# Kernel optimization log

Measured on AMD Instinct MI355X. Metric: run time of the kernel, lower is better.

Reference implementation:

```python
import jax, jax.numpy as jnp
import numpy as np

B, N, D, H, DH, DEPTH, VOCAB, MULT = 4, 1024, 768, 12, 64, 6, 32000, 4
INNER = H * DH
FF = D * MULT
EPS = 1e-6


def setup_inputs() -> dict:
    key = jax.random.key(0)
    ks = jax.random.split(key, 9)
    s = lambda fan: 1.0 / np.sqrt(fan)
    return {
        "tokens": jax.random.randint(ks[0], (B, N), 0, VOCAB, dtype=jnp.int32),
        "mask": jnp.ones((B, N), dtype=bool),
        "embed": jax.random.normal(ks[1], (VOCAB, D), jnp.float32),
        "wq": jax.random.normal(ks[2], (DEPTH, INNER, D), jnp.float32) * s(D),
        "wk": jax.random.normal(ks[3], (DEPTH, INNER, D), jnp.float32) * s(D),
        "wv": jax.random.normal(ks[4], (DEPTH, INNER, D), jnp.float32) * s(D),
        "wo": jax.random.normal(ks[5], (DEPTH, D, INNER), jnp.float32) * s(INNER),
        "wi": jax.random.normal(ks[6], (DEPTH, FF, D), jnp.float32) * s(D),
        "wof": jax.random.normal(ks[7], (DEPTH, D, FF), jnp.float32) * s(FF),
        "ln_w": jnp.ones((D,), jnp.float32),
    }


def _t5_layernorm(x, w):
    var = jnp.mean(jnp.square(x.astype(jnp.float32)), axis=-1, keepdims=True)
    return w * (x * jax.lax.rsqrt(var + EPS))


def reference(tokens, mask, embed, wq, wk, wv, wo, wi, wof, ln_w):
    x = embed[tokens]  # [B, N, D]
    scale = DH ** -0.5
    neg = -jnp.finfo(x.dtype).max
    m = mask[:, None, :, None]  # masks query rows, as in the torch code
    for l in range(DEPTH):
        # attention (no pre-LN: WrapperBlock never calls its layer_norm)
        q = (x @ wq[l].T).reshape(B, N, H, DH).transpose(0, 2, 1, 3) * scale
        k = (x @ wk[l].T).reshape(B, N, H, DH).transpose(0, 2, 1, 3)
        v = (x @ wv[l].T).reshape(B, N, H, DH).transpose(0, 2, 1, 3)
        sim = jnp.einsum('bhid,bhjd->bhij', q, k)
        sim = jnp.where(m, sim, neg)
        attn = jax.nn.softmax(sim, axis=-1)
        o = jnp.einsum('bhij,bhjd->bhid', attn, v)
        o = o.transpose(0, 2, 1, 3).reshape(B, N, INNER) @ wo[l].T
        x = x + o
        # feed-forward
        y = jax.nn.relu(x @ wi[l].T) @ wof[l].T
        x = x + y
    return _t5_layernorm(x, ln_w)
```

## Files before the change

### kernel.cpp

```cpp
#include <hip/hip_runtime.h>
#include <cstdint>

#define NB 4
#define NSEQ 1024
#define DMODEL 768
#define NHEAD 12
#define DHEAD 64
#define NDEPTH 6
#define DFF 3072
#define MROWS (NB * NSEQ)
#define QKVLD 2304

#define WQ_OFF 0L
#define WK_OFF 589824L
#define WV_OFF 1179648L
#define WO_OFF 1769472L
#define WI_OFF 2359296L
#define WOF_OFF 4718592L
#define WTOT 7077888L

typedef __attribute__((ext_vector_type(8))) short short8;
typedef __attribute__((ext_vector_type(4))) float floatx4;

static __device__ __forceinline__ float b2f(unsigned short u) {
  union { unsigned int i; float f; } v; v.i = ((unsigned int)u) << 16; return v.f;
}
static __device__ __forceinline__ unsigned short f2b(float f) {
  union { float f; unsigned int i; } v; v.f = f;
  unsigned int x = v.i;
  return (unsigned short)((x + 0x7fffu + ((x >> 16) & 1u)) >> 16);
}
static __device__ __forceinline__ void fsplit(float f, unsigned short& h, unsigned short& l) {
  h = f2b(f);
  l = f2b(f - b2f(h));
}

static __device__ __forceinline__ void gload16(const unsigned short* g, unsigned short* l) {
  __builtin_amdgcn_global_load_lds(
      (const __attribute__((address_space(1))) void*)g,
      (__attribute__((address_space(3))) void*)l, 16, 0, 0);
}

__global__ __launch_bounds__(256) void wsplit_kernel(
    const float* __restrict__ wq, const float* __restrict__ wk,
    const float* __restrict__ wv, const float* __restrict__ wo,
    const float* __restrict__ wi, const float* __restrict__ wof,
    unsigned short* __restrict__ dhi, unsigned short* __restrict__ dlo)
{
  long i = ((long)blockIdx.x * 256 + threadIdx.x) * 4;
  if (i >= WTOT) return;
  const float* src; long off;
  if (i < WK_OFF)       { src = wq;  off = i - WQ_OFF; }
  else if (i < WV_OFF)  { src = wk;  off = i - WK_OFF; }
  else if (i < WO_OFF)  { src = wv;  off = i - WV_OFF; }
  else if (i < WI_OFF)  { src = wo;  off = i - WO_OFF; }
  else if (i < WOF_OFF) { src = wi;  off = i - WI_OFF; }
  else                  { src = wof; off = i - WOF_OFF; }
  float4 f = *(const float4*)(src + off);
  ushort4 h, l;
  fsplit(f.x, h.x, l.x); fsplit(f.y, h.y, l.y);
  fsplit(f.z, h.z, l.z); fsplit(f.w, h.w, l.w);
  *(ushort4*)(dhi + i) = h;
  *(ushort4*)(dlo + i) = l;
}

__global__ void embed_kernel(const int* __restrict__ tok,
                             const float* __restrict__ emb,
                             unsigned short* __restrict__ xhi,
                             unsigned short* __restrict__ xlo) {
  const int row = blockIdx.x;
  const int t = tok[row];
  const float* src = emb + (long)t * DMODEL;
  for (int d = threadIdx.x; d < DMODEL; d += 256) {
    unsigned short h, l;
    fsplit(src[d], h, l);
    xhi[(long)row * DMODEL + d] = h;
    xlo[(long)row * DMODEL + d] = l;
  }
}

template<int BM, int WGM, int WGN, int MT, int NT, int RELU, int RESID, int QSCALE>
__global__ __launch_bounds__(256) void gemm128(
    const unsigned short* __restrict__ Ahi, const unsigned short* __restrict__ Alo,
    const unsigned short* __restrict__ Whi, const unsigned short* __restrict__ Wlo,
    unsigned short* __restrict__ Chi, unsigned short* __restrict__ Clo,
    const unsigned short* __restrict__ Rhi, const unsigned short* __restrict__ Rlo,
    int N, int K, float alpha)
{
  __shared__ unsigned short sAh[BM * 32];
  __shared__ unsigned short sAl[BM * 32];
  __shared__ unsigned short sBh[128 * 32];
  __shared__ unsigned short sBl[128 * 32];

  const int tid = threadIdx.x;
  const int bn = blockIdx.x, bm = blockIdx.y;
  const int wave = tid >> 6, lane = tid & 63;
  const int wm = wave / WGN, wn = wave % WGN;
  const int l16 = lane & 15, q4 = lane >> 4;

  const int srow = tid >> 2;
  const int scol = (tid & 3) << 3;
  const int soff = tid * 8;

  floatx4 acc[MT][NT];
  #pragma unroll
  for (int i = 0; i < MT; ++i)
    #pragma unroll
    for (int j = 0; j < NT; ++j) {
      floatx4 z = {0.f, 0.f, 0.f, 0.f};
      acc[i][j] = z;
    }

  const long aB = ((long)bm * BM + srow) * K + scol;
  const long bB = ((long)bn * 128 + srow) * K + scol;

  for (int k0 = 0; k0 < K; k0 += 32) {
    #pragma unroll
    for (int c = 0; c < BM / 64; ++c) {
      gload16(Ahi + aB + (long)c * 64 * K + k0, sAh + c * 2048 + soff);
      gload16(Alo + aB + (long)c * 64 * K + k0, sAl + c * 2048 + soff);
    }
    #pragma unroll
    for (int c = 0; c < 2; ++c) {
      gload16(Whi + bB + (long)c * 64 * K + k0, sBh + c * 2048 + soff);
      gload16(Wlo + bB + (long)c * 64 * K + k0, sBl + c * 2048 + soff);
    }
    __syncthreads();

    short8 ah[MT], al[MT], bh[NT], bl[NT];
    #pragma unroll
    for (int mt = 0; mt < MT; ++mt) {
      const int row = wm * (MT * 16) + mt * 16 + l16;
      ah[mt] = *(const short8*)&sAh[row * 32 + q4 * 8];
      al[mt] = *(const short8*)&sAl[row * 32 + q4 * 8];
    }
    #pragma unroll
    for (int nt = 0; nt < NT; ++nt) {
      const int row = wn * (NT * 16) + nt * 16 + l16;
      bh[nt] = *(const short8*)&sBh[row * 32 + q4 * 8];
      bl[nt] = *(const short8*)&sBl[row * 32 + q4 * 8];
    }

    #pragma unroll
    for (int mt = 0; mt < MT; ++mt)
      #pragma unroll
      for (int nt = 0; nt < NT; ++nt)
        acc[mt][nt] = __builtin_amdgcn_mfma_f32_16x16x32_bf16(ah[mt], bh[nt], acc[mt][nt], 0, 0, 0);
    #pragma unroll
    for (int mt = 0; mt < MT; ++mt)
      #pragma unroll
      for (int nt = 0; nt < NT; ++nt)
        acc[mt][nt] = __builtin_amdgcn_mfma_f32_16x16x32_bf16(al[mt], bh[nt], acc[mt][nt], 0, 0, 0);
    #pragma unroll
    for (int mt = 0; mt < MT; ++mt)
      #pragma unroll
      for (int nt = 0; nt < NT; ++nt)
        acc[mt][nt] = __builtin_amdgcn_mfma_f32_16x16x32_bf16(ah[mt], bl[nt], acc[mt][nt], 0, 0, 0);
    __syncthreads();
  }

  #pragma unroll
  for (int mt = 0; mt < MT; ++mt) {
    const int r0 = bm * BM + wm * (MT * 16) + mt * 16 + q4 * 4;
    #pragma unroll
    for (int nt = 0; nt < NT; ++nt) {
      const int c = bn * 128 + wn * (NT * 16) + nt * 16 + l16;
      float sc = alpha;
      if (QSCALE) sc = (c < DMODEL) ? alpha : 1.f;
      #pragma unroll
      for (int r = 0; r < 4; ++r) {
        float vv = acc[mt][nt][r] * sc;
        const long idx = (long)(r0 + r) * N + c;
        if (RESID) vv += b2f(Rhi[idx]) + b2f(Rlo[idx]);
        if (RELU)  vv = fmaxf(vv, 0.f);
        unsigned short h, l;
        fsplit(vv, h, l);
        Chi[idx] = h; Clo[idx] = l;
      }
    }
  }
}

__global__ __launch_bounds__(256) void attn_kernel(
    const unsigned short* __restrict__ qkvhi, const unsigned short* __restrict__ qkvlo,
    unsigned short* __restrict__ ohi, unsigned short* __restrict__ olo)
{
  __shared__ unsigned short ks_h[64][72];
  __shared__ unsigned short ks_l[64][72];
  __shared__ unsigned short vt_h[64][72];
  __shared__ unsigned short vt_l[64][72];
  __shared__ unsigned short ps_h[64][72];
  __shared__ unsigned short ps_l[64][72];

  const int tid = threadIdx.x;
  const int iq = blockIdx.x, h = blockIdx.y, b = blockIdx.z;
  const int wave = tid >> 6, lane = tid & 63;
  const int l16 = lane & 15, g4 = lane >> 4;
  const long qb = ((long)b * NSEQ) * QKVLD + h * DHEAD;
  const long kb = qb + DMODEL;
  const long vb = qb + 2 * DMODEL;
  const long ob = ((long)b * NSEQ) * DMODEL + h * DHEAD;
  const int q0 = iq * 64;

  short8 qh[2], ql[2];
  {
    const long qr = qb + (long)(q0 + wave * 16 + l16) * QKVLD + g4 * 8;
    qh[0] = *(const short8*)(qkvhi + qr);
    qh[1] = *(const short8*)(qkvhi + qr + 32);
    ql[0] = *(const short8*)(qkvlo + qr);
    ql[1] = *(const short8*)(qkvlo + qr + 32);
  }

  floatx4 oacc[4];
  #pragma unroll
  for (int nt = 0; nt < 4; ++nt) { floatx4 z = {0.f,0.f,0.f,0.f}; oacc[nt] = z; }
  float mrow[4] = {-INFINITY, -INFINITY, -INFINITY, -INFINITY};
  float lrow[4] = {0.f, 0.f, 0.f, 0.f};

  const int skey = tid >> 3;
  const int sd0  = (tid & 7) * 8;

  for (int jc = 0; jc < NSEQ / 64; ++jc) {
    const int j0 = jc * 64;
    if (jc) __syncthreads();

    #pragma unroll
    for (int half = 0; half < 2; ++half) {
      const int key = skey + half * 32;
      const long offk = kb + (long)(j0 + key) * QKVLD + sd0;
      const long offv = vb + (long)(j0 + key) * QKVLD + sd0;
      short8 kh8 = *(const short8*)(qkvhi + offk);
      short8 kl8 = *(const short8*)(qkvlo + offk);
      short8 vh8 = *(const short8*)(qkvhi + offv);
      short8 vl8 = *(const short8*)(qkvlo + offv);
      *(short8*)&ks_h[key][sd0] = kh8;
      *(short8*)&ks_l[key][sd0] = kl8;
      #pragma unroll
      for (int u = 0; u < 8; ++u) {
        const int dh = sd0 + u;
        const int cc = key ^ ((dh >> 3) << 3);
        vt_h[dh][cc] = (unsigned short)vh8[u];
        vt_l[dh][cc] = (unsigned short)vl8[u];
      }
    }
    __syncthreads();

    floatx4 sacc[4];
    #pragma unroll
    for (int nt = 0; nt < 4; ++nt) { floatx4 z = {0.f,0.f,0.f,0.f}; sacc[nt] = z; }
    #pragma unroll
    for (int nt = 0; nt < 4; ++nt) {
      #pragma unroll
      for (int ks = 0; ks < 2; ++ks) {
        short8 kh8 = *(const short8*)&ks_h[nt * 16 + l16][ks * 32 + g4 * 8];
        short8 kl8 = *(const short8*)&ks_l[nt * 16 + l16][ks * 32 + g4 * 8];
        sacc[nt] = __builtin_amdgcn_mfma_f32_16x16x32_bf16(qh[ks], kh8, sacc[nt], 0, 0, 0);
        sacc[nt] = __builtin_amdgcn_mfma_f32_16x16x32_bf16(ql[ks], kh8, sacc[nt], 0, 0, 0);
        sacc[nt] = __builtin_amdgcn_mfma_f32_16x16x32_bf16(qh[ks], kl8, sacc[nt], 0, 0, 0);
      }
    }

    float mx[4], al[4];
    #pragma unroll
    for (int r = 0; r < 4; ++r) {
      float m0 = fmaxf(fmaxf(sacc[0][r], sacc[1][r]), fmaxf(sacc[2][r], sacc[3][r]));
      m0 = fmaxf(m0, __shfl_xor(m0, 1));
      m0 = fmaxf(m0, __shfl_xor(m0, 2));
      m0 = fmaxf(m0, __shfl_xor(m0, 4));
      m0 = fmaxf(m0, __shfl_xor(m0, 8));
      const float mn = fmaxf(mrow[r], m0);
      al[r] = __expf(mrow[r] - mn);
      mrow[r] = mn;
      mx[r] = mn;
    }
    #pragma unroll
    for (int r = 0; r < 4; ++r) {
      const int qrow = wave * 16 + g4 * 4 + r;
      float rs = 0.f;
      #pragma unroll
      for (int nt = 0; nt < 4; ++nt) {
        const float p = __expf(sacc[nt][r] - mx[r]);
        rs += p;
        unsigned short ph, pl;
        fsplit(p, ph, pl);
        ps_h[qrow][nt * 16 + l16] = ph;
        ps_l[qrow][nt * 16 + l16] = pl;
      }
      rs += __shfl_xor(rs, 1);
      rs += __shfl_xor(rs, 2);
      rs += __shfl_xor(rs, 4);
      rs += __shfl_xor(rs, 8);
      lrow[r] = lrow[r] * al[r] + rs;
      oacc[0][r] *= al[r]; oacc[1][r] *= al[r];
      oacc[2][r] *= al[r]; oacc[3][r] *= al[r];
    }
    __syncthreads();

    #pragma unroll
    for (int ks = 0; ks < 2; ++ks) {
      short8 ph8 = *(const short8*)&ps_h[wave * 16 + l16][ks * 32 + g4 * 8];
      short8 pl8 = *(const short8*)&ps_l[wave * 16 + l16][ks * 32 + g4 * 8];
      #pragma unroll
      for (int nt = 0; nt < 4; ++nt) {
        const int dh = nt * 16 + l16;
        const int cb = (ks * 32 + g4 * 8) ^ ((dh >> 3) << 3);
        short8 vh8 = *(const short8*)&vt_h[dh][cb];
        short8 vl8 = *(const short8*)&vt_l[dh][cb];
        oacc[nt] = __builtin_amdgcn_mfma_f32_16x16x32_bf16(ph8, vh8, oacc[nt], 0, 0, 0);
        oacc[nt] = __builtin_amdgcn_mfma_f32_16x16x32_bf16(pl8, vh8, oacc[nt], 0, 0, 0);
        oacc[nt] = __builtin_amdgcn_mfma_f32_16x16x32_bf16(ph8, vl8, oacc[nt], 0, 0, 0);
      }
    }
  }

  const long orbase = ob + (long)(q0 + wave * 16 + g4 * 4) * DMODEL;
  #pragma unroll
  for (int r = 0; r < 4; ++r) {
    const float inv = 1.f / lrow[r];
    #pragma unroll
    for (int nt = 0; nt < 4; ++nt) {
      unsigned short hh, ll;
      fsplit(oacc[nt][r] * inv, hh, ll);
      const long idx = orbase + (long)r * DMODEL + nt * 16 + l16;
      ohi[idx] = hh; olo[idx] = ll;
    }
  }
}

__global__ __launch_bounds__(256) void ln_kernel(const unsigned short* __restrict__ xhi,
                                                 const unsigned short* __restrict__ xlo,
                                                 const float* __restrict__ w,
                                                 float* __restrict__ out)
{
  __shared__ float red[256];
  const int row = blockIdx.x;
  const long rb = (long)row * DMODEL;
  float ss = 0.f;
  for (int d = threadIdx.x; d < DMODEL; d += 256) {
    float v = b2f(xhi[rb + d]) + b2f(xlo[rb + d]);
    ss += v * v;
  }
  red[threadIdx.x] = ss;
  __syncthreads();
  for (int s = 128; s > 0; s >>= 1) {
    if (threadIdx.x < s) red[threadIdx.x] += red[threadIdx.x + s];
    __syncthreads();
  }
  const float rs = rsqrtf(red[0] * (1.f / DMODEL) + 1e-6f);
  for (int d = threadIdx.x; d < DMODEL; d += 256) {
    float v = b2f(xhi[rb + d]) + b2f(xlo[rb + d]);
    out[rb + d] = w[d] * v * rs;
  }
}

extern "C" void kernel_launch(void* const* d_in, const int* in_sizes, int n_in,
                              void* d_out, int out_size, void* d_ws, size_t ws_size,
                              hipStream_t stream)
{
  const int* tokens   = (const int*)d_in[0];
  const float* emb    = (const float*)d_in[2];
  const float* wq     = (const float*)d_in[3];
  const float* wk     = (const float*)d_in[4];
  const float* wv     = (const float*)d_in[5];
  const float* wo     = (const float*)d_in[6];
  const float* wi     = (const float*)d_in[7];
  const float* wof    = (const float*)d_in[8];
  const float* lnw    = (const float*)d_in[9];

  const size_t AS = (size_t)MROWS * DMODEL;
  char* p = (char*)d_ws;
  unsigned short* xhi = (unsigned short*)p;  p += AS * 2;
  unsigned short* xlo = (unsigned short*)p;  p += AS * 2;
  unsigned short* act = (unsigned short*)p;  p += AS * 2 * 8;
  unsigned short* whi = (unsigned short*)p;  p += (size_t)WTOT * 2;
  unsigned short* wlo = (unsigned short*)p;  p += (size_t)WTOT * 2;

  unsigned short* qkvhi = act + AS * 0;
  unsigned short* qkvlo = act + AS * 3;
  unsigned short* ohi   = act + AS * 6;
  unsigned short* olo   = act + AS * 7;
  unsigned short* fhi   = act + AS * 0;
  unsigned short* flo   = act + AS * 4;

  embed_kernel<<<MROWS, 256, 0, stream>>>(tokens, emb, xhi, xlo);

  const dim3 gqkv(QKVLD / 128, MROWS / 128);
  const dim3 gwo(DMODEL / 128, MROWS / 64);
  const dim3 gwi(DFF / 128, MROWS / 128);
  const dim3 gattn(NSEQ / 64, NHEAD, NB);
  const int splitblocks = (int)(WTOT / 1024);

  for (int l = 0; l < NDEPTH; ++l) {
    wsplit_kernel<<<splitblocks, 256, 0, stream>>>(
        wq  + (size_t)l * DMODEL * DMODEL,
        wk  + (size_t)l * DMODEL * DMODEL,
        wv  + (size_t)l * DMODEL * DMODEL,
        wo  + (size_t)l * DMODEL * DMODEL,
        wi  + (size_t)l * DFF * DMODEL,
        wof + (size_t)l * DMODEL * DFF,
        whi, wlo);

    gemm128<128,2,2,4,4, 0,0,1><<<gqkv, 256, 0, stream>>>(
        xhi, xlo, whi + WQ_OFF, wlo + WQ_OFF,
        qkvhi, qkvlo, nullptr, nullptr, QKVLD, DMODEL, 0.125f);
    attn_kernel<<<gattn, 256, 0, stream>>>(qkvhi, qkvlo, ohi, olo);
    gemm128<64,1,4,4,2, 0,1,0><<<gwo, 256, 0, stream>>>(
        ohi, olo, whi + WO_OFF, wlo + WO_OFF,
        xhi, xlo, xhi, xlo, DMODEL, DMODEL, 1.f);
    gemm128<128,2,2,4,4, 1,0,0><<<gwi, 256, 0, stream>>>(
        xhi, xlo, whi + WI_OFF, wlo + WI_OFF,
        fhi, flo, nullptr, nullptr, DFF, DMODEL, 1.f);
    gemm128<64,1,4,4,2, 0,1,0><<<gwo, 256, 0, stream>>>(
        fhi, flo, whi + WOF_OFF, wlo + WOF_OFF,
        xhi, xlo, xhi, xlo, DMODEL, DFF, 1.f);
  }

  ln_kernel<<<MROWS, 256, 0, stream>>>(xhi, xlo, lnw, (float*)d_out);
}
```

Before: 2.510 ms.

## Add BK=64 XOR-swizzled K tiling for narrow GEMMs; alias attention P onto K smem

The GEMM template gains a BK parameter. The two N=768 GEMMs (Wo and Wof) now load 64-wide K slices with an XOR swizzle on LDS columns, which halves the number of k-iterations and barriers per tile and avoids bank conflicts. In the attention kernel, the probability tile reuses the K shared buffers. An extra barrier after the QK^T step makes that aliasing safe, and LDS use drops from six arrays to four, which could raise occupancy. The risk is the extra barrier per key chunk and more LDS per GEMM block.

```diff
diff --git a/kernel.cpp b/kernel.cpp
--- a/kernel.cpp
+++ b/kernel.cpp
@@ -79,7 +79,7 @@
   }
 }
 
-template<int BM, int WGM, int WGN, int MT, int NT, int RELU, int RESID, int QSCALE>
+template<int BM, int BK, int WGM, int WGN, int MT, int NT, int RELU, int RESID, int QSCALE>
 __global__ __launch_bounds__(256) void gemm128(
     const unsigned short* __restrict__ Ahi, const unsigned short* __restrict__ Alo,
     const unsigned short* __restrict__ Whi, const unsigned short* __restrict__ Wlo,
@@ -87,10 +87,12 @@
     const unsigned short* __restrict__ Rhi, const unsigned short* __restrict__ Rlo,
     int N, int K, float alpha)
 {
-  __shared__ unsigned short sAh[BM * 32];
-  __shared__ unsigned short sAl[BM * 32];
-  __shared__ unsigned short sBh[128 * 32];
-  __shared__ unsigned short sBl[128 * 32];
+  __shared__ unsigned short sAh[BM * BK];
+  __shared__ unsigned short sAl[BM * BK];
+  __shared__ unsigned short sBh[128 * BK];
+  __shared__ unsigned short sBl[128 * BK];
+
+  constexpr int XM = (BK == 64) ? 7 : 0;
 
   const int tid = threadIdx.x;
   const int bn = blockIdx.x, bm = blockIdx.y;
@@ -98,8 +100,9 @@
   const int wm = wave / WGN, wn = wave % WGN;
   const int l16 = lane & 15, q4 = lane >> 4;
 
-  const int srow = tid >> 2;
-  const int scol = (tid & 3) << 3;
+  constexpr int RPC = 2048 / BK;
+  const int srow = tid / (BK / 8);
+  const int scol = (((tid % (BK / 8)) ^ (srow & XM))) * 8;
   const int soff = tid * 8;
 
   floatx4 acc[MT][NT];
@@ -114,48 +117,53 @@
   const long aB = ((long)bm * BM + srow) * K + scol;
   const long bB = ((long)bn * 128 + srow) * K + scol;
 
-  for (int k0 = 0; k0 < K; k0 += 32) {
-    #pragma unroll
-    for (int c = 0; c < BM / 64; ++c) {
-      gload16(Ahi + aB + (long)c * 64 * K + k0, sAh + c * 2048 + soff);
-      gload16(Alo + aB + (long)c * 64 * K + k0, sAl + c * 2048 + soff);
-    }
-    #pragma unroll
-    for (int c = 0; c < 2; ++c) {
-      gload16(Whi + bB + (long)c * 64 * K + k0, sBh + c * 2048 + soff);
-      gload16(Wlo + bB + (long)c * 64 * K + k0, sBl + c * 2048 + soff);
-    }
-    __syncthreads();
-
-    short8 ah[MT], al[MT], bh[NT], bl[NT];
-    #pragma unroll
-    for (int mt = 0; mt < MT; ++mt) {
-      const int row = wm * (MT * 16) + mt * 16 + l16;
-      ah[mt] = *(const short8*)&sAh[row * 32 + q4 * 8];
-      al[mt] = *(const short8*)&sAl[row * 32 + q4 * 8];
-    }
-    #pragma unroll
-    for (int nt = 0; nt < NT; ++nt) {
-      const int row = wn * (NT * 16) + nt * 16 + l16;
-      bh[nt] = *(const short8*)&sBh[row * 32 + q4 * 8];
-      bl[nt] = *(const short8*)&sBl[row * 32 + q4 * 8];
-    }
-
-    #pragma unroll
-    for (int mt = 0; mt < MT; ++mt)
-      #pragma unroll
-      for (int nt = 0; nt < NT; ++nt)
-        acc[mt][nt] = __builtin_amdgcn_mfma_f32_16x16x32_bf16(ah[mt], bh[nt], acc[mt][nt], 0, 0, 0);
-    #pragma unroll
-    for (int mt = 0; mt < MT; ++mt)
-      #pragma unroll
-      for (int nt = 0; nt < NT; ++nt)
-        acc[mt][nt] = __builtin_amdgcn_mfma_f32_16x16x32_bf16(al[mt], bh[nt], acc[mt][nt], 0, 0, 0);
-    #pragma unroll
-    for (int mt = 0; mt < MT; ++mt)
-      #pragma unroll
-      for (int nt = 0; nt < NT; ++nt)
-        acc[mt][nt] = __builtin_amdgcn_mfma_f32_16x16x32_bf16(ah[mt], bl[nt], acc[mt][nt], 0, 0, 0);
+  for (int k0 = 0; k0 < K; k0 += BK) {
+    #pragma unroll
+    for (int c = 0; c < (BM * BK) / 2048; ++c) {
+      gload16(Ahi + aB + (long)c * RPC * K + k0, sAh + c * 2048 + soff);
+      gload16(Alo + aB + (long)c * RPC * K + k0, sAl + c * 2048 + soff);
+    }
+    #pragma unroll
+    for (int c = 0; c < (128 * BK) / 2048; ++c) {
+      gload16(Whi + bB + (long)c * RPC * K + k0, sBh + c * 2048 + soff);
+      gload16(Wlo + bB + (long)c * RPC * K + k0, sBl + c * 2048 + soff);
+    }
+    __syncthreads();
+
+    #pragma unroll
+    for (int kk = 0; kk < BK / 32; ++kk) {
+      short8 ah[MT], am[MT], bh[NT], bl[NT];
+      #pragma unroll
+      for (int mt = 0; mt < MT; ++mt) {
+        const int row = wm * (MT * 16) + mt * 16 + l16;
+        const int cg  = ((kk * 4 + q4) ^ (row & XM)) * 8;
+        ah[mt] = *(const short8*)&sAh[row * BK + cg];
+        am[mt] = *(const short8*)&sAl[row * BK + cg];
+      }
+      #pragma unroll
+      for (int nt = 0; nt < NT; ++nt) {
+        const int row = wn * (NT * 16) + nt * 16 + l16;
+        const int cg  = ((kk * 4 + q4) ^ (row & XM)) * 8;
+        bh[nt] = *(const short8*)&sBh[row * BK + cg];
+        bl[nt] = *(const short8*)&sBl[row * BK + cg];
+      }
+
+      #pragma unroll
+      for (int mt = 0; mt < MT; ++mt)
+        #pragma unroll
+        for (int nt = 0; nt < NT; ++nt)
+          acc[mt][nt] = __builtin_amdgcn_mfma_f32_16x16x32_bf16(ah[mt], bh[nt], acc[mt][nt], 0, 0, 0);
+      #pragma unroll
+      for (int mt = 0; mt < MT; ++mt)
+        #pragma unroll
+        for (int nt = 0; nt < NT; ++nt)
+          acc[mt][nt] = __builtin_amdgcn_mfma_f32_16x16x32_bf16(am[mt], bh[nt], acc[mt][nt], 0, 0, 0);
+      #pragma unroll
+      for (int mt = 0; mt < MT; ++mt)
+        #pragma unroll
+        for (int nt = 0; nt < NT; ++nt)
+          acc[mt][nt] = __builtin_amdgcn_mfma_f32_16x16x32_bf16(ah[mt], bl[nt], acc[mt][nt], 0, 0, 0);
+    }
     __syncthreads();
   }
 
@@ -185,12 +193,10 @@
     const unsigned short* __restrict__ qkvhi, const unsigned short* __restrict__ qkvlo,
     unsigned short* __restrict__ ohi, unsigned short* __restrict__ olo)
 {
-  __shared__ unsigned short ks_h[64][72];
-  __shared__ unsigned short ks_l[64][72];
+  __shared__ unsigned short kp_h[64][72];
+  __shared__ unsigned short kp_l[64][72];
   __shared__ unsigned short vt_h[64][72];
   __shared__ unsigned short vt_l[64][72];
-  __shared__ unsigned short ps_h[64][72];
-  __shared__ unsigned short ps_l[64][72];
 
   const int tid = threadIdx.x;
   const int iq = blockIdx.x, h = blockIdx.y, b = blockIdx.z;
@@ -233,8 +239,8 @@
       short8 kl8 = *(const short8*)(qkvlo + offk);
       short8 vh8 = *(const short8*)(qkvhi + offv);
       short8 vl8 = *(const short8*)(qkvlo + offv);
-      *(short8*)&ks_h[key][sd0] = kh8;
-      *(short8*)&ks_l[key][sd0] = kl8;
+      *(short8*)&kp_h[key][sd0] = kh8;
+      *(short8*)&kp_l[key][sd0] = kl8;
       #pragma unroll
       for (int u = 0; u < 8; ++u) {
         const int dh = sd0 + u;
@@ -252,13 +258,14 @@
     for (int nt = 0; nt < 4; ++nt) {
       #pragma unroll
       for (int ks = 0; ks < 2; ++ks) {
-        short8 kh8 = *(const short8*)&ks_h[nt * 16 + l16][ks * 32 + g4 * 8];
-        short8 kl8 = *(const short8*)&ks_l[nt * 16 + l16][ks * 32 + g4 * 8];
+        short8 kh8 = *(const short8*)&kp_h[nt * 16 + l16][ks * 32 + g4 * 8];
+        short8 kl8 = *(const short8*)&kp_l[nt * 16 + l16][ks * 32 + g4 * 8];
         sacc[nt] = __builtin_amdgcn_mfma_f32_16x16x32_bf16(qh[ks], kh8, sacc[nt], 0, 0, 0);
         sacc[nt] = __builtin_amdgcn_mfma_f32_16x16x32_bf16(ql[ks], kh8, sacc[nt], 0, 0, 0);
         sacc[nt] = __builtin_amdgcn_mfma_f32_16x16x32_bf16(qh[ks], kl8, sacc[nt], 0, 0, 0);
       }
     }
+    __syncthreads();
 
     float mx[4], al[4];
     #pragma unroll
@@ -283,8 +290,8 @@
         rs += p;
         unsigned short ph, pl;
         fsplit(p, ph, pl);
-        ps_h[qrow][nt * 16 + l16] = ph;
-        ps_l[qrow][nt * 16 + l16] = pl;
+        kp_h[qrow][nt * 16 + l16] = ph;
+        kp_l[qrow][nt * 16 + l16] = pl;
       }
       rs += __shfl_xor(rs, 1);
       rs += __shfl_xor(rs, 2);
@@ -298,8 +305,8 @@
 
     #pragma unroll
     for (int ks = 0; ks < 2; ++ks) {
-      short8 ph8 = *(const short8*)&ps_h[wave * 16 + l16][ks * 32 + g4 * 8];
-      short8 pl8 = *(const short8*)&ps_l[wave * 16 + l16][ks * 32 + g4 * 8];
+      short8 ph8 = *(const short8*)&kp_h[wave * 16 + l16][ks * 32 + g4 * 8];
+      short8 pl8 = *(const short8*)&kp_l[wave * 16 + l16][ks * 32 + g4 * 8];
       #pragma unroll
       for (int nt = 0; nt < 4; ++nt) {
         const int dh = nt * 16 + l16;
@@ -400,17 +407,17 @@
         wof + (size_t)l * DMODEL * DFF,
         whi, wlo);
 
-    gemm128<128,2,2,4,4, 0,0,1><<<gqkv, 256, 0, stream>>>(
+    gemm128<128,32,2,2,4,4, 0,0,1><<<gqkv, 256, 0, stream>>>(
         xhi, xlo, whi + WQ_OFF, wlo + WQ_OFF,
         qkvhi, qkvlo, nullptr, nullptr, QKVLD, DMODEL, 0.125f);
     attn_kernel<<<gattn, 256, 0, stream>>>(qkvhi, qkvlo, ohi, olo);
-    gemm128<64,1,4,4,2, 0,1,0><<<gwo, 256, 0, stream>>>(
+    gemm128<64,64,1,4,4,2, 0,1,0><<<gwo, 256, 0, stream>>>(
         ohi, olo, whi + WO_OFF, wlo + WO_OFF,
         xhi, xlo, xhi, xlo, DMODEL, DMODEL, 1.f);
-    gemm128<128,2,2,4,4, 1,0,0><<<gwi, 256, 0, stream>>>(
+    gemm128<128,32,2,2,4,4, 1,0,0><<<gwi, 256, 0, stream>>>(
         xhi, xlo, whi + WI_OFF, wlo + WI_OFF,
         fhi, flo, nullptr, nullptr, DFF, DMODEL, 1.f);
-    gemm128<64,1,4,4,2, 0,1,0><<<gwo, 256, 0, stream>>>(
+    gemm128<64,64,1,4,4,2, 0,1,0><<<gwo, 256, 0, stream>>>(
         fhi, flo, whi + WOF_OFF, wlo + WOF_OFF,
         xhi, xlo, xhi, xlo, DMODEL, DFF, 1.f);
   }
```

Result: faster. 2.293 ms (-8.7%).
